# Optimization experiments

Measured on AMD Instinct MI355X. Metric: run time of the kernel, lower is better.

## Reference

```python
import jax, jax.numpy as jnp
import numpy as np

NUM_HEADS = 16


def setup_inputs() -> dict:
    key = jax.random.key(0)
    k1, k2, k3, k4 = jax.random.split(key, 4)
    B, N, D = 4, 2048, 1024
    inputs = jax.random.normal(k1, (B, N, D), dtype=jnp.float32)
    w_in = jax.random.normal(k2, (3 * D, D), dtype=jnp.float32) * (D ** -0.5)
    w_out = jax.random.normal(k3, (D, D), dtype=jnp.float32) * (D ** -0.5)
    b_out = jax.random.normal(k4, (D,), dtype=jnp.float32) * 0.02
    return {"inputs": inputs, "w_in": w_in, "w_out": w_out, "b_out": b_out}


def reference(inputs, w_in, w_out, b_out):
    B, N, D = inputs.shape
    H = NUM_HEADS
    Hd = D // H
    # in_proj (torch Linear: x @ W.T), split into Q,K,V
    qkv = jnp.einsum('bnd,ed->bne', inputs, w_in)  # [B,N,3D]
    q, k, v = jnp.split(qkv, 3, axis=-1)
    # [B,H,N,Hd]
    q = q.reshape(B, N, H, Hd).transpose(0, 2, 1, 3)
    k = k.reshape(B, N, H, Hd).transpose(0, 2, 1, 3)
    v = v.reshape(B, N, H, Hd).transpose(0, 2, 1, 3)
    scores = jnp.einsum('bhqd,bhkd->bhqk', q, k) * (Hd ** -0.5)
    causal = jnp.triu(jnp.ones((N, N), dtype=bool), k=1)  # True above diagonal
    scores = jnp.where(causal, -jnp.inf, scores)
    attn = jax.nn.softmax(scores, axis=-1)
    out = jnp.einsum('bhqk,bhkd->bhqd', attn, v)  # [B,H,N,Hd]
    out = out.transpose(0, 2, 1, 3).reshape(B, N, D)
    return jnp.einsum('bnd,ed->bne', out, w_out) + b_out
```

## Files before the change

### kernel.cpp

```cpp
#include <hip/hip_runtime.h>
#include <hip/hip_bf16.h>
#include <cstdint>

typedef __hip_bfloat16 bf16;
typedef short short8 __attribute__((ext_vector_type(8)));
typedef float f32x4 __attribute__((ext_vector_type(4)));

#define AS1C(p) ((const __attribute__((address_space(1))) void*)(p))
#define AS3(p)  ((__attribute__((address_space(3))) void*)(p))

__device__ __forceinline__ float b2f(short s) {
    union { unsigned u; float f; } c; c.u = ((unsigned)(unsigned short)s) << 16; return c.f;
}

template<int CTRL>
__device__ __forceinline__ float dppf(float x) {
    return __int_as_float(__builtin_amdgcn_update_dpp(
        0, __float_as_int(x), CTRL, 0xF, 0xF, true));
}
__device__ __forceinline__ float row_sum16(float x) {
    x += dppf<0xB1>(x);
    x += dppf<0x4E>(x);
    x += dppf<0x141>(x);
    x += dppf<0x140>(x);
    return x;
}

#define N4_X  2097152
#define N4_WI  786432
#define N4_WO  262144
__global__ void cvt_all(const float* __restrict__ x, bf16* __restrict__ xb,
                        const float* __restrict__ wi, bf16* __restrict__ wib,
                        const float* __restrict__ wo, bf16* __restrict__ wob)
{
    int i = blockIdx.x * blockDim.x + threadIdx.x;
    const float* src; bf16* dst; int off;
    if (i < N4_X)                { src = x;  dst = xb;  off = i; }
    else if (i < N4_X + N4_WI)   { src = wi; dst = wib; off = i - N4_X; }
    else                         { src = wo; dst = wob; off = i - N4_X - N4_WI; }
    float4 v = ((const float4*)src)[off];
    __align__(8) bf16 t[4] = { __float2bfloat16(v.x), __float2bfloat16(v.y),
                               __float2bfloat16(v.z), __float2bfloat16(v.w) };
    ((uint2*)dst)[off] = *(const uint2*)t;
}

template<bool SPLIT_V, bool HAS_BIAS, typename OUT_T>
__global__ __launch_bounds__(512, 2)
void gemm_8ph(const bf16* __restrict__ A, int lda, const bf16* __restrict__ B,
              const float* __restrict__ bias, OUT_T* __restrict__ C, int ldc,
              bf16* __restrict__ vt, int K)
{
    __shared__ __align__(16) bf16 As[2][2][8192];
    __shared__ __align__(16) bf16 Bs[2][2][8192];
    const int tid  = threadIdx.x;
    const int wave = tid >> 6, lane = tid & 63;
    const int wm = wave >> 2, wn = wave & 3;
    const int quad = lane >> 4, l15 = lane & 15;
    const int tile_m = blockIdx.x, tile_n = blockIdx.y;

    const bf16* Ap = A + (size_t)tile_m * 256 * lda;
    const bf16* Bp = B + (size_t)tile_n * 256 * K;
    const int srow = lane >> 2;
    const int scol = (lane & 3) * 8;
    const int fo   = l15 * 32 + quad * 8;

    f32x4 acc[2][2][4][2];
    #pragma unroll
    for (int a = 0; a < 2; a++)
        #pragma unroll
        for (int b = 0; b < 2; b++)
            #pragma unroll
            for (int m = 0; m < 4; m++)
                #pragma unroll
                for (int n = 0; n < 2; n++) acc[a][b][m][n] = (f32x4){0.f,0.f,0.f,0.f};

    #define STA(T, H)                                                              \
        {   const int k0_ = (T) * 64, s_ = (T) & 1;                                \
            _Pragma("unroll")                                                      \
            for (int i = 0; i < 2; i++) {                                          \
                int u = wave * 2 + i, c = u >> 1, kh = u & 1;                      \
                const bf16* g = Ap + (size_t)((H) * 128 + c * 16 + srow) * lda     \
                              + k0_ + kh * 32 + scol;                              \
                __builtin_amdgcn_global_load_lds(AS1C(g),                          \
                    AS3(&As[s_][H][u * 512]), 16, 0, 0);                           \
            }                                                                      \
        }
    #define STB(T, H)                                                              \
        {   const int k0_ = (T) * 64, s_ = (T) & 1;                                \
            _Pragma("unroll")                                                      \
            for (int i = 0; i < 2; i++) {                                          \
                int u = wave * 2 + i, c = u >> 1, kh = u & 1;                      \
                const bf16* g = Bp + (size_t)((H) * 128 + c * 16 + srow) * K       \
                              + k0_ + kh * 32 + scol;                              \
                __builtin_amdgcn_global_load_lds(AS1C(g),                          \
                    AS3(&Bs[s_][H][u * 512]), 16, 0, 0);                           \
            }                                                                      \
        }
    #define LGK() { asm volatile("s_waitcnt lgkmcnt(0)" ::: "memory");             \
                    __builtin_amdgcn_sched_barrier(0); }
    #define MFMA_PHASE(QM, QN)                                                     \
        __builtin_amdgcn_s_setprio(1);                                             \
        _Pragma("unroll")                                                          \
        for (int kh = 0; kh < 2; kh++)                                             \
            _Pragma("unroll")                                                      \
            for (int mi = 0; mi < 4; mi++)                                         \
                _Pragma("unroll")                                                  \
                for (int ni = 0; ni < 2; ni++)                                     \
                    acc[QM][QN][mi][ni] = __builtin_amdgcn_mfma_f32_16x16x32_bf16( \
                        af[mi][kh], bq[QN][ni][kh], acc[QM][QN][mi][ni], 0, 0, 0); \
        __builtin_amdgcn_s_setprio(0);

    const int nk = K >> 6;
    STA(0, 0) STB(0, 0) STA(0, 1) STB(0, 1)
    STA(1, 0) STB(1, 0)
    asm volatile("s_waitcnt vmcnt(4)" ::: "memory");
    __builtin_amdgcn_s_barrier();

    for (int t = 0; t < nk; ++t) {
        const int s = t & 1;
        short8 af[4][2];
        short8 bq[2][2][2];

        #pragma unroll
        for (int mi = 0; mi < 4; mi++)
            #pragma unroll
            for (int kh = 0; kh < 2; kh++)
                af[mi][kh] = *(const short8*)&As[s][0][((wm*4+mi)*2+kh)*512 + fo];
        #pragma unroll
        for (int ni = 0; ni < 2; ni++)
            #pragma unroll
            for (int kh = 0; kh < 2; kh++)
                bq[0][ni][kh] = *(const short8*)&Bs[s][0][((wn*2+ni)*2+kh)*512 + fo];
        if (t + 1 < nk) STA(t + 1, 1)
        __builtin_amdgcn_s_barrier();
        LGK()
        MFMA_PHASE(0, 0)
        __builtin_amdgcn_s_barrier();

        #pragma unroll
        for (int ni = 0; ni < 2; ni++)
            #pragma unroll
            for (int kh = 0; kh < 2; kh++)
                bq[1][ni][kh] = *(const short8*)&Bs[s][1][((wn*2+ni)*2+kh)*512 + fo];
        if (t + 1 < nk) STB(t + 1, 1)
        __builtin_amdgcn_s_barrier();
        LGK()
        MFMA_PHASE(0, 1)
        __builtin_amdgcn_s_barrier();

        #pragma unroll
        for (int mi = 0; mi < 4; mi++)
            #pragma unroll
            for (int kh = 0; kh < 2; kh++)
                af[mi][kh] = *(const short8*)&As[s][1][((wm*4+mi)*2+kh)*512 + fo];
        if (t + 2 < nk) STA(t + 2, 0)
        __builtin_amdgcn_s_barrier();
        LGK()
        MFMA_PHASE(1, 0)
        __builtin_amdgcn_s_barrier();

        if (t + 2 < nk) {
            asm volatile("s_waitcnt vmcnt(2)" ::: "memory");
            STB(t + 2, 0)
        } else {
            asm volatile("s_waitcnt vmcnt(0)" ::: "memory");
        }
        __builtin_amdgcn_s_barrier();
        MFMA_PHASE(1, 1)
        __builtin_amdgcn_s_barrier();
    }
    #undef STA
    #undef STB
    #undef LGK
    #undef MFMA_PHASE

    const bool vtile = SPLIT_V && (tile_n * 256 >= 2048);
    #pragma unroll
    for (int qm = 0; qm < 2; qm++) {
        #pragma unroll
        for (int qn = 0; qn < 2; qn++) {
            #pragma unroll
            for (int mi = 0; mi < 4; mi++) {
                #pragma unroll
                for (int ni = 0; ni < 2; ni++) {
                    int coln = tile_n * 256 + qn * 128 + wn * 32 + ni * 16 + l15;
                    int row0 = tile_m * 256 + qm * 128 + wm * 64 + mi * 16 + quad * 4;
                    if (!vtile) {
                        float bv = HAS_BIAS ? bias[coln] : 0.f;
                        #pragma unroll
                        for (int r = 0; r < 4; r++) {
                            float v = acc[qm][qn][mi][ni][r] + bv;
                            if constexpr (__is_same(OUT_T, float))
                                C[(size_t)(row0 + r) * ldc + coln] = v;
                            else
                                C[(size_t)(row0 + r) * ldc + coln] = __float2bfloat16(v);
                        }
                    } else {
                        int vcol = coln - 2048;
                        int bb = row0 >> 11, n0 = row0 & 2047;
                        __align__(8) bf16 t4[4];
                        #pragma unroll
                        for (int r = 0; r < 4; r++)
                            t4[r] = __float2bfloat16(acc[qm][qn][mi][ni][r]);
                        *(uint2*)&vt[((size_t)(bb * 1024 + vcol)) * 2048 + n0] =
                            *(const uint2*)t4;
                    }
                }
            }
        }
    }
}

template<int TM, bool HAS_BIAS, typename OUT_T>
__global__ __launch_bounds__(TM * 2)
void gemm_bt(const bf16* __restrict__ A, int lda, const bf16* __restrict__ B,
             const float* __restrict__ bias, OUT_T* __restrict__ C, int ldc,
             int K)
{
    constexpr int NWAVE = TM / 32;
    __shared__ __align__(16) bf16 As[2][TM * 32];
    __shared__ __align__(16) bf16 Bs[2][128 * 32];
    const int tid  = threadIdx.x;
    const int wave = tid >> 6, lane = tid & 63;
    const int wm = wave >> 1, wn = wave & 1;
    const int quad = lane >> 4, l15 = lane & 15;
    const int tile_m = blockIdx.x, tile_n = blockIdx.y;

    const bf16* Ap = A + (size_t)tile_m * TM * lda;
    const bf16* Bp = B + (size_t)tile_n * 128 * K;

    const int srow = lane >> 2;
    const int scol = (lane & 3) * 8;

    f32x4 acc[4][4];
    #pragma unroll
    for (int i = 0; i < 4; i++)
        #pragma unroll
        for (int j = 0; j < 4; j++) acc[i][j] = (f32x4){0.f, 0.f, 0.f, 0.f};

    #define GSTAGE(KI, BUF)                                                        \
        {   const int k0_ = (KI) * 32;                                             \
            _Pragma("unroll")                                                      \
            for (int cc = 0; cc < 2; cc++) {                                       \
                int c = wave + cc * NWAVE;                                         \
                const bf16* ga = Ap + (size_t)(c * 16 + srow) * lda + k0_ + scol;  \
                __builtin_amdgcn_global_load_lds(AS1C(ga),                         \
                    AS3(&As[BUF][c * 16 * 32]), 16, 0, 0);                         \
            }                                                                      \
            _Pragma("unroll")                                                      \
            for (int cc = 0; cc < 8 / NWAVE; cc++) {                               \
                int c = wave + cc * NWAVE;                                         \
                const bf16* gb = Bp + (size_t)(c * 16 + srow) * K + k0_ + scol;    \
                __builtin_amdgcn_global_load_lds(AS1C(gb),                         \
                    AS3(&Bs[BUF][c * 16 * 32]), 16, 0, 0);                         \
            }                                                                      \
        }

    const int nk = K >> 5;
    GSTAGE(0, 0)
    for (int ki = 0; ki < nk; ki++) {
        __syncthreads();
        const int buf = ki & 1;
        if (ki + 1 < nk) GSTAGE(ki + 1, buf ^ 1)

        short8 af[4], bfr[4];
        #pragma unroll
        for (int mi = 0; mi < 4; mi++)
            af[mi] = *(const short8*)&As[buf][(wm * 64 + mi * 16 + l15) * 32 + quad * 8];
        #pragma unroll
        for (int ni = 0; ni < 4; ni++)
            bfr[ni] = *(const short8*)&Bs[buf][(wn * 64 + ni * 16 + l15) * 32 + quad * 8];
        #pragma unroll
        for (int mi = 0; mi < 4; mi++)
            #pragma unroll
            for (int ni = 0; ni < 4; ni++)
                acc[mi][ni] = __builtin_amdgcn_mfma_f32_16x16x32_bf16(
                    af[mi], bfr[ni], acc[mi][ni], 0, 0, 0);
    }
    #undef GSTAGE

    #pragma unroll
    for (int mi = 0; mi < 4; mi++) {
        #pragma unroll
        for (int ni = 0; ni < 4; ni++) {
            int coln = tile_n * 128 + wn * 64 + ni * 16 + l15;
            float bv = HAS_BIAS ? bias[coln] : 0.f;
            #pragma unroll
            for (int r = 0; r < 4; r++) {
                int row = tile_m * TM + wm * 64 + mi * 16 + quad * 4 + r;
                float v = acc[mi][ni][r] + bv;
                if constexpr (__is_same(OUT_T, float))
                    C[(size_t)row * ldc + coln] = v;
                else
                    C[(size_t)row * ldc + coln] = __float2bfloat16(v);
            }
        }
    }
}

__global__ __launch_bounds__(256, 3)
void flash_attn(bf16* __restrict__ qkv, const bf16* __restrict__ vt)
{
    const int idx = blockIdx.x;
    const int qt  = 15 - (idx >> 6);
    const int bh  = idx & 63;
    const int b   = bh >> 4, h = bh & 15;
    const int tid = threadIdx.x;
    const int wave = tid >> 6, lane = tid & 63;
    const int quad = lane >> 4, l15 = lane & 15;

    __shared__ __align__(16) bf16 Ks[2][64 * 64];
    __shared__ __align__(16) bf16 Vs[2][64 * 64];
    __shared__ __align__(16) bf16 Ps[4][2][16][72];

    const int q0   = qt * 128;
    const int rowA = wave * 32;
    const size_t rs = 2048;

    const float QSC = 0.18033688011112042f;
    short8 qa[2][2];
    #pragma unroll
    for (int mi = 0; mi < 2; mi++)
        #pragma unroll
        for (int kw = 0; kw < 2; kw++) {
            const bf16* qr = qkv + (size_t)(b * 2048 + q0 + rowA + mi * 16 + l15) * rs
                           + h * 64 + kw * 32 + quad * 8;
            short8 t = *(const short8*)qr;
            #pragma unroll
            for (int e = 0; e < 8; e++)
                t[e] = (short)__bfloat16_as_ushort(__float2bfloat16(b2f(t[e]) * QSC));
            qa[mi][kw] = t;
        }

    f32x4 o[2][4];
    #pragma unroll
    for (int mi = 0; mi < 2; mi++)
        #pragma unroll
        for (int nt = 0; nt < 4; nt++) o[mi][nt] = (f32x4){0.f, 0.f, 0.f, 0.f};
    float lsum[2][4] = {{0.f,0.f,0.f,0.f},{0.f,0.f,0.f,0.f}};

    const bf16* kbase = qkv + (size_t)(b * 2048) * rs + 1024 + h * 64;
    const bf16* vbase = vt + (size_t)(bh * 64) * 2048;

    const int srow8  = lane >> 3;
    const int schunk = (lane & 7) ^ srow8;

    #define STAGE(J, BUF)                                                          \
        {   const int jj = (J);                                                    \
            _Pragma("unroll")                                                      \
            for (int i = 0; i < 2; i++) {                                          \
                int rr_ = wave * 16 + i * 8 + srow8;                               \
                const bf16* gk = kbase + (size_t)(jj * 64 + rr_) * rs + schunk * 8;\
                __builtin_amdgcn_global_load_lds(AS1C(gk),                         \
                    AS3(&Ks[BUF][(wave * 16 + i * 8) * 64]), 16, 0, 0);            \
                const bf16* gv = vbase + (size_t)rr_ * 2048 + jj * 64 + schunk * 8;\
                __builtin_amdgcn_global_load_lds(AS1C(gv),                         \
                    AS3(&Vs[BUF][(wave * 16 + i * 8) * 64]), 16, 0, 0);            \
            }                                                                      \
        }

    STAGE(0, 0)
    const int jmax = 2 * qt + 1;
    for (int j = 0; j <= jmax; j++) {
        __syncthreads();
        const int buf = j & 1;
        if (j < jmax) STAGE(j + 1, buf ^ 1)

        if (j * 64 > q0 + rowA + 31) continue;

        f32x4 s[2][4];
        #pragma unroll
        for (int mi = 0; mi < 2; mi++)
            #pragma unroll
            for (int tc = 0; tc < 4; tc++) s[mi][tc] = (f32x4){0.f,0.f,0.f,0.f};
        #pragma unroll
        for (int kw = 0; kw < 2; kw++) {
            short8 kb[4];
            #pragma unroll
            for (int tc = 0; tc < 4; tc++)
                kb[tc] = *(const short8*)&Ks[buf][(tc * 16 + l15) * 64 +
                         (((kw * 4 + quad) ^ (l15 & 7)) * 8)];
            #pragma unroll
            for (int mi = 0; mi < 2; mi++)
                #pragma unroll
                for (int tc = 0; tc < 4; tc++)
                    s[mi][tc] = __builtin_amdgcn_mfma_f32_16x16x32_bf16(
                        qa[mi][kw], kb[tc], s[mi][tc], 0, 0, 0);
        }
        if (j * 64 + 63 > q0 + rowA) {
            #pragma unroll
            for (int mi = 0; mi < 2; mi++)
                #pragma unroll
                for (int tc = 0; tc < 4; tc++)
                    #pragma unroll
                    for (int rr = 0; rr < 4; rr++)
                        if (j * 64 + tc * 16 + l15 >
                            q0 + rowA + mi * 16 + quad * 4 + rr)
                            s[mi][tc][rr] = -INFINITY;
        }
        #pragma unroll
        for (int mi = 0; mi < 2; mi++) {
            #pragma unroll
            for (int tc = 0; tc < 4; tc++)
                #pragma unroll
                for (int rr = 0; rr < 4; rr++)
                    s[mi][tc][rr] = __builtin_amdgcn_exp2f(s[mi][tc][rr]);
            #pragma unroll
            for (int rr = 0; rr < 4; rr++)
                lsum[mi][rr] += (s[mi][0][rr] + s[mi][1][rr]) +
                                (s[mi][2][rr] + s[mi][3][rr]);
        }
        #pragma unroll
        for (int mi = 0; mi < 2; mi++)
            #pragma unroll
            for (int tc = 0; tc < 4; tc++)
                #pragma unroll
                for (int rr = 0; rr < 4; rr++)
                    Ps[wave][mi][quad * 4 + rr][tc * 16 + l15] =
                        __float2bfloat16(s[mi][tc][rr]);
        #pragma unroll
        for (int kw = 0; kw < 2; kw++) {
            short8 vb[4];
            #pragma unroll
            for (int nt = 0; nt < 4; nt++)
                vb[nt] = *(const short8*)&Vs[buf][(nt * 16 + l15) * 64 +
                         (((kw * 4 + quad) ^ (l15 & 7)) * 8)];
            short8 pa[2];
            #pragma unroll
            for (int mi = 0; mi < 2; mi++)
                pa[mi] = *(const short8*)&Ps[wave][mi][l15][kw * 32 + quad * 8];
            #pragma unroll
            for (int mi = 0; mi < 2; mi++)
                #pragma unroll
                for (int nt = 0; nt < 4; nt++)
                    o[mi][nt] = __builtin_amdgcn_mfma_f32_16x16x32_bf16(
                        pa[mi], vb[nt], o[mi][nt], 0, 0, 0);
        }
    }
    #undef STAGE

    #pragma unroll
    for (int mi = 0; mi < 2; mi++)
        #pragma unroll
        for (int rr = 0; rr < 4; rr++) {
            float inv = 1.f / row_sum16(lsum[mi][rr]);
            int row = b * 2048 + q0 + rowA + mi * 16 + quad * 4 + rr;
            #pragma unroll
            for (int nt = 0; nt < 4; nt++) {
                int col = h * 64 + nt * 16 + l15;
                qkv[(size_t)row * rs + col] = __float2bfloat16(o[mi][nt][rr] * inv);
            }
        }
}

extern "C" void kernel_launch(void* const* d_in, const int* in_sizes, int n_in,
                              void* d_out, int out_size, void* d_ws, size_t ws_size,
                              hipStream_t stream)
{
    const float* x     = (const float*)d_in[0];
    const float* w_in  = (const float*)d_in[1];
    const float* w_out = (const float*)d_in[2];
    const float* b_out = (const float*)d_in[3];
    float* out = (float*)d_out;

    bf16* qkv = (bf16*)d_ws;
    bf16* vt  = qkv + (size_t)8192 * 2048;
    bf16* xb  = vt  + (size_t)4096 * 2048;
    bf16* wib = xb  + (size_t)8192 * 1024;
    bf16* wob = wib + (size_t)3072 * 1024;

    cvt_all<<<(N4_X + N4_WI + N4_WO) / 256, 256, 0, stream>>>(
        x, xb, w_in, wib, w_out, wob);

    gemm_8ph<true, false, bf16><<<dim3(8192 / 256, 3072 / 256), 512, 0, stream>>>(
        xb, 1024, wib, nullptr, qkv, 2048, vt, 1024);
    flash_attn<<<1024, 256, 0, stream>>>(qkv, vt);
    gemm_bt<128, true, float><<<dim3(8192 / 128, 1024 / 128), 256, 0, stream>>>(
        qkv, 2048, wob, b_out, out, 1024, 1024);
}
```

Measured before the change: 248.0 us.

## Rework LDS fragment layouts, transpose QK^T in attention, and enlarge out-proj tile

Each GEMM now stages each 16x32 fragment so that lane*8 addresses it contiguously, which changes the global-to-LDS load mapping and the LDS read indexing. In attention, the QK^T MFMA swaps its operands so the score tile is transposed. That lets P be written to LDS with one packed 8-byte store, and the row sum is reduced with shuffles instead of DPP. MFMA sections are wrapped in s_setprio. The output projection moves to a 256-row tile with 512 threads, and gemm_bt gains an unused V-split path. Together these aim to cut LDS bank conflicts and store counts, at the cost of larger per-block register and LDS footprints.

```diff
diff --git a/kernel.cpp b/kernel.cpp
--- a/kernel.cpp
+++ b/kernel.cpp
@@ -11,19 +11,6 @@
 
 __device__ __forceinline__ float b2f(short s) {
     union { unsigned u; float f; } c; c.u = ((unsigned)(unsigned short)s) << 16; return c.f;
-}
-
-template<int CTRL>
-__device__ __forceinline__ float dppf(float x) {
-    return __int_as_float(__builtin_amdgcn_update_dpp(
-        0, __float_as_int(x), CTRL, 0xF, 0xF, true));
-}
-__device__ __forceinline__ float row_sum16(float x) {
-    x += dppf<0xB1>(x);
-    x += dppf<0x4E>(x);
-    x += dppf<0x141>(x);
-    x += dppf<0x140>(x);
-    return x;
 }
 
 #define N4_X  2097152
@@ -60,9 +47,9 @@
 
     const bf16* Ap = A + (size_t)tile_m * 256 * lda;
     const bf16* Bp = B + (size_t)tile_n * 256 * K;
-    const int srow = lane >> 2;
-    const int scol = (lane & 3) * 8;
-    const int fo   = l15 * 32 + quad * 8;
+    const int srow = lane & 15;
+    const int scol = (lane >> 4) * 8;
+    const int fo   = lane * 8;
 
     f32x4 acc[2][2][4][2];
     #pragma unroll
@@ -211,11 +198,11 @@
     }
 }
 
-template<int TM, bool HAS_BIAS, typename OUT_T>
+template<int TM, bool SPLIT_V, bool HAS_BIAS, typename OUT_T>
 __global__ __launch_bounds__(TM * 2)
 void gemm_bt(const bf16* __restrict__ A, int lda, const bf16* __restrict__ B,
              const float* __restrict__ bias, OUT_T* __restrict__ C, int ldc,
-             int K)
+             bf16* __restrict__ vt, int M, int N, int K)
 {
     constexpr int NWAVE = TM / 32;
     __shared__ __align__(16) bf16 As[2][TM * 32];
@@ -229,8 +216,8 @@
     const bf16* Ap = A + (size_t)tile_m * TM * lda;
     const bf16* Bp = B + (size_t)tile_n * 128 * K;
 
-    const int srow = lane >> 2;
-    const int scol = (lane & 3) * 8;
+    const int srow = lane & 15;
+    const int scol = (lane >> 4) * 8;
 
     f32x4 acc[4][4];
     #pragma unroll
@@ -241,14 +228,14 @@
     #define GSTAGE(KI, BUF)                                                        \
         {   const int k0_ = (KI) * 32;                                             \
             _Pragma("unroll")                                                      \
-            for (int cc = 0; cc < 2; cc++) {                                       \
+            for (int cc = 0; cc < 2; cc++) {                  \
                 int c = wave + cc * NWAVE;                                         \
                 const bf16* ga = Ap + (size_t)(c * 16 + srow) * lda + k0_ + scol;  \
                 __builtin_amdgcn_global_load_lds(AS1C(ga),                         \
                     AS3(&As[BUF][c * 16 * 32]), 16, 0, 0);                         \
             }                                                                      \
             _Pragma("unroll")                                                      \
-            for (int cc = 0; cc < 8 / NWAVE; cc++) {                               \
+            for (int cc = 0; cc < 8 / NWAVE; cc++) {              \
                 int c = wave + cc * NWAVE;                                         \
                 const bf16* gb = Bp + (size_t)(c * 16 + srow) * K + k0_ + scol;    \
                 __builtin_amdgcn_global_load_lds(AS1C(gb),                         \
@@ -266,10 +253,10 @@
         short8 af[4], bfr[4];
         #pragma unroll
         for (int mi = 0; mi < 4; mi++)
-            af[mi] = *(const short8*)&As[buf][(wm * 64 + mi * 16 + l15) * 32 + quad * 8];
+            af[mi] = *(const short8*)&As[buf][(wm * 4 + mi) * 512 + lane * 8];
         #pragma unroll
         for (int ni = 0; ni < 4; ni++)
-            bfr[ni] = *(const short8*)&Bs[buf][(wn * 64 + ni * 16 + l15) * 32 + quad * 8];
+            bfr[ni] = *(const short8*)&Bs[buf][(wn * 4 + ni) * 512 + lane * 8];
         #pragma unroll
         for (int mi = 0; mi < 4; mi++)
             #pragma unroll
@@ -279,20 +266,31 @@
     }
     #undef GSTAGE
 
+    const bool vtile = SPLIT_V && (tile_n * 128 >= 2048);
     #pragma unroll
     for (int mi = 0; mi < 4; mi++) {
         #pragma unroll
         for (int ni = 0; ni < 4; ni++) {
             int coln = tile_n * 128 + wn * 64 + ni * 16 + l15;
-            float bv = HAS_BIAS ? bias[coln] : 0.f;
-            #pragma unroll
-            for (int r = 0; r < 4; r++) {
-                int row = tile_m * TM + wm * 64 + mi * 16 + quad * 4 + r;
-                float v = acc[mi][ni][r] + bv;
-                if constexpr (__is_same(OUT_T, float))
-                    C[(size_t)row * ldc + coln] = v;
-                else
-                    C[(size_t)row * ldc + coln] = __float2bfloat16(v);
+            if (!vtile) {
+                float bv = HAS_BIAS ? bias[coln] : 0.f;
+                #pragma unroll
+                for (int r = 0; r < 4; r++) {
+                    int row = tile_m * TM + wm * 64 + mi * 16 + quad * 4 + r;
+                    float v = acc[mi][ni][r] + bv;
+                    if constexpr (__is_same(OUT_T, float))
+                        C[(size_t)row * ldc + coln] = v;
+                    else
+                        C[(size_t)row * ldc + coln] = __float2bfloat16(v);
+                }
+            } else {
+                int vcol = coln - 2048;
+                int row0 = tile_m * TM + wm * 64 + mi * 16 + quad * 4;
+                int bb = row0 >> 11, n0 = row0 & 2047;
+                __align__(8) bf16 t4[4];
+                #pragma unroll
+                for (int r = 0; r < 4; r++) t4[r] = __float2bfloat16(acc[mi][ni][r]);
+                *(uint2*)&vt[((size_t)(bb * 1024 + vcol)) * 2048 + n0] = *(const uint2*)t4;
             }
         }
     }
@@ -337,7 +335,7 @@
     for (int mi = 0; mi < 2; mi++)
         #pragma unroll
         for (int nt = 0; nt < 4; nt++) o[mi][nt] = (f32x4){0.f, 0.f, 0.f, 0.f};
-    float lsum[2][4] = {{0.f,0.f,0.f,0.f},{0.f,0.f,0.f,0.f}};
+    float lsum[2] = {0.f, 0.f};
 
     const bf16* kbase = qkv + (size_t)(b * 2048) * rs + 1024 + h * 64;
     const bf16* vbase = vt + (size_t)(bh * 64) * 2048;
@@ -380,12 +378,14 @@
             for (int tc = 0; tc < 4; tc++)
                 kb[tc] = *(const short8*)&Ks[buf][(tc * 16 + l15) * 64 +
                          (((kw * 4 + quad) ^ (l15 & 7)) * 8)];
+            __builtin_amdgcn_s_setprio(1);
             #pragma unroll
             for (int mi = 0; mi < 2; mi++)
                 #pragma unroll
                 for (int tc = 0; tc < 4; tc++)
                     s[mi][tc] = __builtin_amdgcn_mfma_f32_16x16x32_bf16(
-                        qa[mi][kw], kb[tc], s[mi][tc], 0, 0, 0);
+                        kb[tc], qa[mi][kw], s[mi][tc], 0, 0, 0);
+            __builtin_amdgcn_s_setprio(0);
         }
         if (j * 64 + 63 > q0 + rowA) {
             #pragma unroll
@@ -394,8 +394,8 @@
                 for (int tc = 0; tc < 4; tc++)
                     #pragma unroll
                     for (int rr = 0; rr < 4; rr++)
-                        if (j * 64 + tc * 16 + l15 >
-                            q0 + rowA + mi * 16 + quad * 4 + rr)
+                        if (j * 64 + tc * 16 + quad * 4 + rr >
+                            q0 + rowA + mi * 16 + l15)
                             s[mi][tc][rr] = -INFINITY;
         }
         #pragma unroll
@@ -406,18 +406,21 @@
                 for (int rr = 0; rr < 4; rr++)
                     s[mi][tc][rr] = __builtin_amdgcn_exp2f(s[mi][tc][rr]);
             #pragma unroll
-            for (int rr = 0; rr < 4; rr++)
-                lsum[mi][rr] += (s[mi][0][rr] + s[mi][1][rr]) +
-                                (s[mi][2][rr] + s[mi][3][rr]);
+            for (int tc = 0; tc < 4; tc++)
+                lsum[mi] += (s[mi][tc][0] + s[mi][tc][1]) +
+                            (s[mi][tc][2] + s[mi][tc][3]);
         }
         #pragma unroll
         for (int mi = 0; mi < 2; mi++)
             #pragma unroll
-            for (int tc = 0; tc < 4; tc++)
+            for (int tc = 0; tc < 4; tc++) {
+                __align__(8) bf16 t4[4];
                 #pragma unroll
                 for (int rr = 0; rr < 4; rr++)
-                    Ps[wave][mi][quad * 4 + rr][tc * 16 + l15] =
-                        __float2bfloat16(s[mi][tc][rr]);
+                    t4[rr] = __float2bfloat16(s[mi][tc][rr]);
+                *(uint2*)&Ps[wave][mi][l15][tc * 16 + quad * 4] =
+                    *(const uint2*)t4;
+            }
         #pragma unroll
         for (int kw = 0; kw < 2; kw++) {
             short8 vb[4];
@@ -429,26 +432,38 @@
             #pragma unroll
             for (int mi = 0; mi < 2; mi++)
                 pa[mi] = *(const short8*)&Ps[wave][mi][l15][kw * 32 + quad * 8];
+            __builtin_amdgcn_s_setprio(1);
             #pragma unroll
             for (int mi = 0; mi < 2; mi++)
                 #pragma unroll
                 for (int nt = 0; nt < 4; nt++)
                     o[mi][nt] = __builtin_amdgcn_mfma_f32_16x16x32_bf16(
                         pa[mi], vb[nt], o[mi][nt], 0, 0, 0);
+            __builtin_amdgcn_s_setprio(0);
         }
     }
     #undef STAGE
 
+    float inv[2][4];
+    #pragma unroll
+    for (int mi = 0; mi < 2; mi++) {
+        float t = lsum[mi];
+        t += __shfl_xor(t, 16);
+        t += __shfl_xor(t, 32);
+        #pragma unroll
+        for (int rr = 0; rr < 4; rr++)
+            inv[mi][rr] = 1.f / __shfl(t, quad * 4 + rr);
+    }
     #pragma unroll
     for (int mi = 0; mi < 2; mi++)
         #pragma unroll
         for (int rr = 0; rr < 4; rr++) {
-            float inv = 1.f / row_sum16(lsum[mi][rr]);
             int row = b * 2048 + q0 + rowA + mi * 16 + quad * 4 + rr;
             #pragma unroll
             for (int nt = 0; nt < 4; nt++) {
                 int col = h * 64 + nt * 16 + l15;
-                qkv[(size_t)row * rs + col] = __float2bfloat16(o[mi][nt][rr] * inv);
+                qkv[(size_t)row * rs + col] =
+                    __float2bfloat16(o[mi][nt][rr] * inv[mi][rr]);
             }
         }
 }
@@ -475,6 +490,6 @@
     gemm_8ph<true, false, bf16><<<dim3(8192 / 256, 3072 / 256), 512, 0, stream>>>(
         xb, 1024, wib, nullptr, qkv, 2048, vt, 1024);
     flash_attn<<<1024, 256, 0, stream>>>(qkv, vt);
-    gemm_bt<128, true, float><<<dim3(8192 / 128, 1024 / 128), 256, 0, stream>>>(
-        qkv, 2048, wob, b_out, out, 1024, 1024);
-}
+    gemm_bt<256, false, true, float><<<dim3(8192 / 256, 1024 / 128), 512, 0, stream>>>(
+        qkv, 2048, wob, b_out, out, 1024, nullptr, 8192, 1024, 1024);
+}
```

After: 267.6 us. 7.9% more time.
